# Kernel tuning notes

Hardware: AMD Instinct MI355X
Metric: run time of the kernel (lower is better)

The kernel has to match this reference:

```python
import jax, jax.numpy as jnp
import numpy as np

N = 100000
E = 1600000
DIN = 128
DH = 128
DOUT = 32
G = 64
EPS = 1e-5


def setup_inputs() -> dict:
    key = jax.random.key(0)
    ks = jax.random.split(key, 12)
    x = jax.random.normal(ks[0], (N, DIN), dtype=jnp.float32)
    edge_index = jax.random.randint(ks[1], (2, E), 0, N, dtype=jnp.int64)
    batch = jnp.sort(jax.random.randint(ks[2], (N,), 0, G, dtype=jnp.int64))
    # GCNConv weights (glorot-ish) + zero bias
    W1 = jax.random.normal(ks[3], (DIN, DH), dtype=jnp.float32) * (2.0 / (DIN + DH)) ** 0.5
    b1 = jnp.zeros((DH,), jnp.float32)
    W2 = jax.random.normal(ks[4], (DH, DH), dtype=jnp.float32) * (2.0 / (DH + DH)) ** 0.5
    b2 = jnp.zeros((DH,), jnp.float32)
    # BatchNorm affine params
    g1 = jnp.ones((DH,), jnp.float32); be1 = jnp.zeros((DH,), jnp.float32)
    g2 = jnp.ones((DH,), jnp.float32); be2 = jnp.zeros((DH,), jnp.float32)
    # Linear heads: kaiming normal fan_in relu, bias=0.001
    fw1 = jax.random.normal(ks[5], (DH, DH), dtype=jnp.float32) * (2.0 / DH) ** 0.5
    fb1 = jnp.full((DH,), 0.001, jnp.float32)
    fw2 = jax.random.normal(ks[6], (DH, DOUT), dtype=jnp.float32) * (2.0 / DH) ** 0.5
    fb2 = jnp.full((DOUT,), 0.001, jnp.float32)
    return dict(x=x, edge_index=edge_index, batch=batch, W1=W1, b1=b1, W2=W2, b2=b2,
                g1=g1, be1=be1, g2=g2, be2=be2, fw1=fw1, fb1=fb1, fw2=fw2, fb2=fb2)


def _gcn(x, src, dst, dinv, W, b):
    h = x @ W  # [N, F]
    norm = dinv[src] * dinv[dst]  # [E+N]
    agg = jax.ops.segment_sum(h[src] * norm[:, None], dst, num_segments=N)
    return agg + b


def _bn(h, gamma, beta):
    mu = h.mean(axis=0)
    var = h.var(axis=0)  # biased, matches torch BN training mode
    return (h - mu) * jax.lax.rsqrt(var + EPS) * gamma + beta


def reference(x, edge_index, batch, W1, b1, W2, b2, g1, be1, g2, be2, fw1, fb1, fw2, fb2):
    # add self-loops (PyG GCNConv default)
    loops = jnp.arange(N, dtype=edge_index.dtype)
    src = jnp.concatenate([edge_index[0], loops])
    dst = jnp.concatenate([edge_index[1], loops])
    deg = jax.ops.segment_sum(jnp.ones_like(dst, dtype=x.dtype), dst, num_segments=N)
    dinv = jnp.where(deg > 0, jax.lax.rsqrt(deg), 0.0)

    h = jax.nn.relu(_bn(_gcn(x, src, dst, dinv, W1, b1), g1, be1))
    h = jax.nn.relu(_bn(_gcn(h, src, dst, dinv, W2, b2), g2, be2))

    # global mean pool over graph ids
    sums = jax.ops.segment_sum(h, batch, num_segments=G)
    cnt = jax.ops.segment_sum(jnp.ones((N,), h.dtype), batch, num_segments=G)
    pooled = sums / jnp.maximum(cnt, 1.0)[:, None]  # [G, DH]

    z = jax.nn.relu(pooled @ fw1 + fb1)
    return jax.nn.softmax(z @ fw2 + fb2, axis=1)
```

## Files before the change

### kernel.cpp

```cpp
#include <hip/hip_runtime.h>
#include <hip/hip_bf16.h>
#include <stdint.h>

#define NN 100000
#define NE 1600000
#define DH 128
#define DOUT 32
#define NG 64
#define EPS 1e-5f

#define SCAN_BLK 1024
#define SCAN_NB ((NN + SCAN_BLK - 1) / SCAN_BLK)
#define NBUCKET 32
#define NRANGE 8
#define RANGE_SZ (NN / NRANGE)

#define PREP_COUNT_BLKS 1024
#define PREP_GB_BLKS ((NN + 255) / 256)
#define PREP_PW_BLKS 128

#define AGG_BLOCKS 4096
#define NCHUNK 32768

typedef __attribute__((ext_vector_type(8))) unsigned short ushort8;
typedef __attribute__((ext_vector_type(8))) short bfv8;
typedef __attribute__((ext_vector_type(4))) float f32x4;
typedef __attribute__((ext_vector_type(4))) int intv4;
typedef __attribute__((ext_vector_type(2))) unsigned int uintv2;

__device__ __forceinline__ float b2f(unsigned short u) {
    return __uint_as_float(((unsigned int)u) << 16);
}
__device__ __forceinline__ unsigned int f2b(float f) {
    unsigned int u = __float_as_uint(f);
    return (u + 0x7fffu + ((u >> 16) & 1u)) >> 16;
}
__device__ __forceinline__ float blo(unsigned int v) { return __uint_as_float(v << 16); }
__device__ __forceinline__ float bhi(unsigned int v) { return __uint_as_float(v & 0xffff0000u); }


__global__ void k_prep(const int* __restrict__ ei_dst, int* __restrict__ cnt,
                       const int* __restrict__ batch, int* __restrict__ gfirst, int* __restrict__ glast,
                       const float* __restrict__ W1, const float* __restrict__ W2,
                       unsigned short* __restrict__ WT1, unsigned short* __restrict__ WT2) {
    int bid = blockIdx.x;
    int t = threadIdx.x;
    if (bid < PREP_COUNT_BLKS) {
        int range = bid & (NRANGE - 1);
        int lo = range * RANGE_SZ, hi = lo + RANGE_SZ;
        int i = (bid >> 3) * 256 + t;
        int stride = (PREP_COUNT_BLKS >> 3) * 256;
        const intv4* d4 = reinterpret_cast<const intv4*>(ei_dst);
        for (int e = i; e < NE / 4; e += stride) {
            intv4 d = __builtin_nontemporal_load(d4 + e);
            if (d.x >= lo && d.x < hi) atomicAdd(&cnt[d.x], 1);
            if (d.y >= lo && d.y < hi) atomicAdd(&cnt[d.y], 1);
            if (d.z >= lo && d.z < hi) atomicAdd(&cnt[d.z], 1);
            if (d.w >= lo && d.w < hi) atomicAdd(&cnt[d.w], 1);
        }
    } else if (bid < PREP_COUNT_BLKS + PREP_GB_BLKS) {
        int i = (bid - PREP_COUNT_BLKS) * 256 + t;
        if (i < NN) {
            int g = batch[i];
            if (i == 0 || batch[i - 1] != g) gfirst[g] = i;
            if (i == NN - 1 || batch[i + 1] != g) glast[g] = i + 1;
        }
    } else {
        int i = (bid - PREP_COUNT_BLKS - PREP_GB_BLKS) * 256 + t;
        int sel = i >> 14;
        int j = i & 16383;
        int k = j >> 7, n = j & 127;
        const float* W = sel ? W2 : W1;
        unsigned short* WT = sel ? WT2 : WT1;
        WT[n * 128 + k] = (unsigned short)f2b(W[j]);
    }
}


__global__ void k_scan_partial(const int* __restrict__ cnt, int* __restrict__ bsum) {
    __shared__ int sdata[256];
    int blk = blockIdx.x, t = threadIdx.x;
    int base = blk * SCAN_BLK + t * 4;
    int s = 0;
#pragma unroll
    for (int q = 0; q < 4; q++) { int idx = base + q; if (idx < NN) s += cnt[idx]; }
    sdata[t] = s; __syncthreads();
    for (int o = 128; o; o >>= 1) { if (t < o) sdata[t] += sdata[t + o]; __syncthreads(); }
    if (t == 0) bsum[blk] = sdata[0];
}

__global__ void k_scan_final(int* __restrict__ cnt, const int* __restrict__ bsum,
                             int* __restrict__ rowptr, float* __restrict__ dinv,
                             const int* __restrict__ first, const int* __restrict__ last,
                             int* __restrict__ gcnt) {
    __shared__ int sdata[256];
    __shared__ int stop[128];
    __shared__ int sbase;
    int blk = blockIdx.x, t = threadIdx.x;

    if (t < 128) stop[t] = (t < SCAN_NB) ? bsum[t] : 0;
    __syncthreads();
    for (int o = 1; o < 128; o <<= 1) {
        int add = (t < 128 && t >= o) ? stop[t - o] : 0;
        __syncthreads();
        if (t < 128) stop[t] += add;
        __syncthreads();
    }
    if (t == 0) sbase = (blk > 0) ? stop[blk - 1] : 0;
    if (blk == 0) {
        if (t == 127) rowptr[NN] = stop[127];
        if (t < NG) gcnt[t] = last[t] - first[t];
    }
    __syncthreads();

    int base = blk * SCAN_BLK + t * 4;
    int v[4]; int s = 0;
#pragma unroll
    for (int q = 0; q < 4; q++) { int idx = base + q; v[q] = (idx < NN) ? cnt[idx] : 0; s += v[q]; }
    sdata[t] = s; __syncthreads();
    for (int o = 1; o < 256; o <<= 1) {
        int add = (t >= o) ? sdata[t - o] : 0;
        __syncthreads();
        sdata[t] += add;
        __syncthreads();
    }
    int offset = sbase + sdata[t] - s;
#pragma unroll
    for (int q = 0; q < 4; q++) {
        int idx = base + q;
        if (idx < NN) {
            rowptr[idx] = offset;
            cnt[idx] = offset;
            dinv[idx] = rsqrtf((float)(v[q] + 1));
            offset += v[q];
        }
    }
}

__global__ void k_fill(const int* __restrict__ ei, int* __restrict__ cursor, int* __restrict__ csr) {
    int range = blockIdx.x & (NRANGE - 1);
    int lo = range * RANGE_SZ, hi = lo + RANGE_SZ;
    int i = (blockIdx.x >> 3) * blockDim.x + threadIdx.x;
    int stride = (gridDim.x >> 3) * blockDim.x;
    const intv4* s4 = reinterpret_cast<const intv4*>(ei);
    const intv4* d4 = reinterpret_cast<const intv4*>(ei + NE);
    for (int e = i; e < NE / 4; e += stride) {
        intv4 s = __builtin_nontemporal_load(s4 + e);
        intv4 d = __builtin_nontemporal_load(d4 + e);
        if (d.x >= lo && d.x < hi) csr[atomicAdd(&cursor[d.x], 1)] = s.x;
        if (d.y >= lo && d.y < hi) csr[atomicAdd(&cursor[d.y], 1)] = s.y;
        if (d.z >= lo && d.z < hi) csr[atomicAdd(&cursor[d.z], 1)] = s.z;
        if (d.w >= lo && d.w < hi) csr[atomicAdd(&cursor[d.w], 1)] = s.w;
    }
}


template <bool BN, typename AT>
__global__ __launch_bounds__(256) void k_gemm(const AT* __restrict__ A, const unsigned short* __restrict__ WTg,
                                              unsigned short* __restrict__ C, const float* __restrict__ rowscale,
                                              const float* __restrict__ scale, const float* __restrict__ shift) {
    __shared__ unsigned char lds[65536];
    unsigned char* As = lds;
    unsigned char* Ws = lds + 32768;
    int row0 = blockIdx.x * 128;
    int t = threadIdx.x;
    int l = t & 63;
    int w = t >> 6;

    if constexpr (sizeof(AT) == 4) {
#pragma unroll
        for (int q = 0; q < 16; q++) {
            int idx = q * 256 + t;
            int r = idx >> 5, c4 = idx & 31;
            float4 v = make_float4(0.f, 0.f, 0.f, 0.f);
            if (row0 + r < NN) v = reinterpret_cast<const float4*>(A)[(size_t)(row0 + r) * 32 + c4];
            ushort4 u;
            u.x = (unsigned short)f2b(v.x);
            u.y = (unsigned short)f2b(v.y);
            u.z = (unsigned short)f2b(v.z);
            u.w = (unsigned short)f2b(v.w);
            int off = r * 256 + ((c4 * 8) ^ ((r & 7) << 4));
            *reinterpret_cast<ushort4*>(As + off) = u;
        }
    } else {
#pragma unroll
        for (int q = 0; q < 8; q++) {
            int idx = q * 256 + t;
            int r = idx >> 4, c8 = idx & 15;
            ushort8 v = (ushort8)0;
            if (row0 + r < NN) v = reinterpret_cast<const ushort8*>(A)[(size_t)(row0 + r) * 16 + c8];
            ushort8 u;
#pragma unroll
            for (int j = 0; j < 8; j++) {
                float f = b2f(v[j]);
                if (BN) { int k = c8 * 8 + j; f = fmaxf(f * scale[k] + shift[k], 0.f); }
                u[j] = (unsigned short)f2b(f);
            }
            int off = r * 256 + ((c8 * 16) ^ ((r & 7) << 4));
            *reinterpret_cast<ushort8*>(As + off) = u;
        }
    }
#pragma unroll
    for (int q = 0; q < 8; q++) {
        int idx = q * 256 + t;
        int n = idx >> 4, c8 = idx & 15;
        ushort8 v = reinterpret_cast<const ushort8*>(WTg)[idx];
        int off = n * 256 + ((c8 * 16) ^ ((n & 7) << 4));
        *reinterpret_cast<ushort8*>(Ws + off) = v;
    }
    __syncthreads();

    f32x4 acc[2][8];
#pragma unroll
    for (int m = 0; m < 2; m++)
#pragma unroll
        for (int n = 0; n < 8; n++) acc[m][n] = (f32x4)0.f;

    int lrow = l & 15;
    int kbyte0 = (l >> 4) * 16;
#pragma unroll
    for (int kt = 0; kt < 4; kt++) {
        int kb = kt * 64 + kbyte0;
        bfv8 a[2];
#pragma unroll
        for (int m = 0; m < 2; m++) {
            int r = w * 32 + m * 16 + lrow;
            a[m] = *reinterpret_cast<const bfv8*>(As + r * 256 + (kb ^ ((r & 7) << 4)));
        }
        bfv8 b[8];
#pragma unroll
        for (int n = 0; n < 8; n++) {
            int r = n * 16 + lrow;
            b[n] = *reinterpret_cast<const bfv8*>(Ws + r * 256 + (kb ^ ((r & 7) << 4)));
        }
#pragma unroll
        for (int m = 0; m < 2; m++)
#pragma unroll
            for (int n = 0; n < 8; n++)
                acc[m][n] = __builtin_amdgcn_mfma_f32_16x16x32_bf16(a[m], b[n], acc[m][n], 0, 0, 0);
    }

#pragma unroll
    for (int m = 0; m < 2; m++) {
#pragma unroll
        for (int rr = 0; rr < 4; rr++) {
            int grow = row0 + w * 32 + m * 16 + (l >> 4) * 4 + rr;
            if (grow < NN) {
                float rs = rowscale[grow];
#pragma unroll
                for (int n = 0; n < 8; n++) {
                    int col = n * 16 + (l & 15);
                    C[(size_t)grow * DH + col] = (unsigned short)f2b(acc[m][n][rr] * rs);
                }
            }
        }
    }
}


__global__ __launch_bounds__(128) void k_aggregate(const unsigned short* __restrict__ h, const int* __restrict__ rowptr,
                                                   const int* __restrict__ csr, const float* __restrict__ dinv,
                                                   unsigned short* __restrict__ agg, float* __restrict__ stats) {
    int lane = threadIdx.x & 63;
    int wv = threadIdx.x >> 6;
    int half = lane >> 5;
    int sl = lane & 31;
    const uintv2* h64 = reinterpret_cast<const uintv2*>(h);
    uintv2* agg64 = reinterpret_cast<uintv2*>(agg);
    int wid = blockIdx.x * 2 + wv;
    int nw = gridDim.x * 2;

    float s0 = 0.f, s1 = 0.f, s2 = 0.f, s3 = 0.f;
    float q0 = 0.f, q1 = 0.f, q2 = 0.f, q3 = 0.f;

    for (int c = wid; c < NCHUNK; c += nw) {
        long long tlo = ((long long)c * NE) / NCHUNK;
        long long thi = (c == NCHUNK - 1) ? (long long)NE + 1 : (((long long)(c + 1) * NE) / NCHUNK);
        int thii = (int)thi;

        int lo = 0, hi = NN;
        while (lo < hi) {
            int mid = (lo + hi) >> 1;
            if (rowptr[mid] < (int)tlo) lo = mid + 1; else hi = mid;
        }

        for (int i = lo; i < NN; i++) {
            int row = rowptr[i];
            if (row >= thii) break;
            int end = rowptr[i + 1];
            int len = end - row;
            float di = dinv[i];
            float a0 = 0.f, a1 = 0.f, a2 = 0.f, a3 = 0.f;
            if (half == 0) {
                uintv2 sv = h64[(size_t)i * 32 + sl];
                a0 = blo(sv.x); a1 = bhi(sv.x); a2 = blo(sv.y); a3 = bhi(sv.y);
            }
            int hc = (len + 1 - half) >> 1;
            int tt = 0;
            for (; tt + 4 <= hc; tt += 4) {
                int eA = row + (tt << 1) + half;
                int n0 = csr[eA], n1 = csr[eA + 2], n2 = csr[eA + 4], n3 = csr[eA + 6];
                uintv2 v0 = h64[(size_t)n0 * 32 + sl];
                uintv2 v1 = h64[(size_t)n1 * 32 + sl];
                uintv2 v2 = h64[(size_t)n2 * 32 + sl];
                uintv2 v3 = h64[(size_t)n3 * 32 + sl];
                a0 += blo(v0.x); a1 += bhi(v0.x); a2 += blo(v0.y); a3 += bhi(v0.y);
                a0 += blo(v1.x); a1 += bhi(v1.x); a2 += blo(v1.y); a3 += bhi(v1.y);
                a0 += blo(v2.x); a1 += bhi(v2.x); a2 += blo(v2.y); a3 += bhi(v2.y);
                a0 += blo(v3.x); a1 += bhi(v3.x); a2 += blo(v3.y); a3 += bhi(v3.y);
            }
            for (; tt < hc; tt++) {
                int e = row + (tt << 1) + half;
                int n = csr[e];
                uintv2 v = h64[(size_t)n * 32 + sl];
                a0 += blo(v.x); a1 += bhi(v.x); a2 += blo(v.y); a3 += bhi(v.y);
            }
            a0 += __shfl_xor(a0, 32);
            a1 += __shfl_xor(a1, 32);
            a2 += __shfl_xor(a2, 32);
            a3 += __shfl_xor(a3, 32);
            a0 *= di; a1 *= di; a2 *= di; a3 *= di;
            if (half == 0) {
                uintv2 o;
                o.x = f2b(a0) | (f2b(a1) << 16);
                o.y = f2b(a2) | (f2b(a3) << 16);
                agg64[(size_t)i * 32 + sl] = o;
                s0 += a0; q0 += a0 * a0;
                s1 += a1; q1 += a1 * a1;
                s2 += a2; q2 += a2 * a2;
                s3 += a3; q3 += a3 * a3;
            }
        }
    }

    if (half == 0) {
        float* b = stats + (size_t)(wid & (NBUCKET - 1)) * 256;
        atomicAdd(&b[sl * 4 + 0], s0);
        atomicAdd(&b[sl * 4 + 1], s1);
        atomicAdd(&b[sl * 4 + 2], s2);
        atomicAdd(&b[sl * 4 + 3], s3);
        atomicAdd(&b[128 + sl * 4 + 0], q0);
        atomicAdd(&b[128 + sl * 4 + 1], q1);
        atomicAdd(&b[128 + sl * 4 + 2], q2);
        atomicAdd(&b[128 + sl * 4 + 3], q3);
    }
}

__global__ void k_bnparams(const float* __restrict__ stats, const float* __restrict__ gamma,
                           const float* __restrict__ beta, float* __restrict__ scale, float* __restrict__ shift) {
    int j = threadIdx.x;
    float su = 0.f, sq = 0.f;
    for (int b = 0; b < NBUCKET; b++) { su += stats[b * 256 + j]; sq += stats[b * 256 + 128 + j]; }
    float mu = su * (1.f / NN);
    float var = sq * (1.f / NN) - mu * mu;
    float rs = rsqrtf(var + EPS);
    float sc = rs * gamma[j];
    scale[j] = sc;
    shift[j] = beta[j] - mu * sc;
}


#define POOL_CHUNK 256

__global__ __launch_bounds__(256) void k_pool(const unsigned short* __restrict__ agg, const int* __restrict__ batch,
                                              const float* __restrict__ stats, const float* __restrict__ gamma,
                                              const float* __restrict__ beta, float* __restrict__ pooled) {
    __shared__ float s_sc[DH], s_sh[DH];
    int t = threadIdx.x;
    if (t < DH) {
        float su = 0.f, sq = 0.f;
        for (int b = 0; b < NBUCKET; b++) { su += stats[b * 256 + t]; sq += stats[b * 256 + 128 + t]; }
        float mu = su * (1.f / NN);
        float var = sq * (1.f / NN) - mu * mu;
        float rs = rsqrtf(var + EPS);
        float sc = rs * gamma[t];
        s_sc[t] = sc;
        s_sh[t] = beta[t] - mu * sc;
    }
    __syncthreads();

    int half = t >> 5;
    int sl = t & 31;
    int n0 = blockIdx.x * POOL_CHUNK + half * 32;
    if (n0 >= NN) return;
    int n1 = n0 + 32; if (n1 > NN) n1 = NN;

    const uintv2* a64 = reinterpret_cast<const uintv2*>(agg);
    float sc0 = s_sc[sl * 4 + 0], sh0 = s_sh[sl * 4 + 0];
    float sc1 = s_sc[sl * 4 + 1], sh1 = s_sh[sl * 4 + 1];
    float sc2 = s_sc[sl * 4 + 2], sh2 = s_sh[sl * 4 + 2];
    float sc3 = s_sc[sl * 4 + 3], sh3 = s_sh[sl * 4 + 3];

    int gcur = batch[n0];
    float a0 = 0.f, a1 = 0.f, a2 = 0.f, a3 = 0.f;
    for (int i = n0; i < n1; i++) {
        int g = batch[i];
        if (g != gcur) {
            atomicAdd(&pooled[(size_t)gcur * DH + sl * 4 + 0], a0);
            atomicAdd(&pooled[(size_t)gcur * DH + sl * 4 + 1], a1);
            atomicAdd(&pooled[(size_t)gcur * DH + sl * 4 + 2], a2);
            atomicAdd(&pooled[(size_t)gcur * DH + sl * 4 + 3], a3);
            a0 = a1 = a2 = a3 = 0.f; gcur = g;
        }
        uintv2 v = a64[(size_t)i * 32 + sl];
        a0 += fmaxf(blo(v.x) * sc0 + sh0, 0.f);
        a1 += fmaxf(bhi(v.x) * sc1 + sh1, 0.f);
        a2 += fmaxf(blo(v.y) * sc2 + sh2, 0.f);
        a3 += fmaxf(bhi(v.y) * sc3 + sh3, 0.f);
    }
    atomicAdd(&pooled[(size_t)gcur * DH + sl * 4 + 0], a0);
    atomicAdd(&pooled[(size_t)gcur * DH + sl * 4 + 1], a1);
    atomicAdd(&pooled[(size_t)gcur * DH + sl * 4 + 2], a2);
    atomicAdd(&pooled[(size_t)gcur * DH + sl * 4 + 3], a3);
}


__global__ __launch_bounds__(128) void k_head(const float* __restrict__ pooled, const int* __restrict__ gcnt,
                                              const float* __restrict__ fw1, const float* __restrict__ fb1,
                                              const float* __restrict__ fw2, const float* __restrict__ fb2,
                                              float* __restrict__ out) {
    __shared__ float p[DH];
    __shared__ float z[DH];
    int g = blockIdx.x;
    int j = threadIdx.x;
    float cnt = (float)max(gcnt[g], 1);
    p[j] = pooled[(size_t)g * DH + j] / cnt;
    __syncthreads();
    float a = fb1[j];
    for (int k = 0; k < DH; k++) a += p[k] * fw1[k * DH + j];
    z[j] = fmaxf(a, 0.f);
    __syncthreads();
    if (j < DOUT) {
        float l = fb2[j];
        for (int k = 0; k < DH; k++) l += z[k] * fw2[k * DOUT + j];
        float m = l;
        for (int o = 16; o; o >>= 1) m = fmaxf(m, __shfl_xor(m, o, 32));
        float e = expf(l - m);
        float s = e;
        for (int o = 16; o; o >>= 1) s += __shfl_xor(s, o, 32);
        out[(size_t)g * DOUT + j] = e / s;
    }
}


static inline char* align256p(char* p) {
    return (char*)(((uintptr_t)p + 255) & ~(uintptr_t)255);
}

extern "C" void kernel_launch(void* const* d_in, const int* in_sizes, int n_in,
                              void* d_out, int out_size, void* d_ws, size_t ws_size,
                              hipStream_t stream) {
    const float* x     = (const float*)d_in[0];
    const int*   ei    = (const int*)d_in[1];
    const int*   batch = (const int*)d_in[2];
    const float* W1    = (const float*)d_in[3];
    const float* W2    = (const float*)d_in[5];
    const float* g1    = (const float*)d_in[7];
    const float* be1   = (const float*)d_in[8];
    const float* g2    = (const float*)d_in[9];
    const float* be2   = (const float*)d_in[10];
    const float* fw1   = (const float*)d_in[11];
    const float* fb1   = (const float*)d_in[12];
    const float* fw2   = (const float*)d_in[13];
    const float* fb2   = (const float*)d_in[14];
    float* out = (float*)d_out;

    char* w = (char*)d_ws;
    unsigned short* hbuf = (unsigned short*)w;  w += (size_t)NN * DH * 2;
    unsigned short* abuf = (unsigned short*)w;  w += (size_t)NN * DH * 2;
    int*   csr    = (int*)w;    w += (size_t)NE * 4;
    int*   rowptr = (int*)w;    w += (size_t)(NN + 1) * 4;  w = align256p(w);
    float* dinv   = (float*)w;  w += (size_t)NN * 4;
    int*   bsum   = (int*)w;    w += 512 * 4;
    float* scale1 = (float*)w;  w += DH * 4;
    float* shift1 = (float*)w;  w += DH * 4;
    unsigned short* WT1g = (unsigned short*)w;  w += (size_t)DH * DH * 2;
    unsigned short* WT2g = (unsigned short*)w;  w += (size_t)DH * DH * 2;
    w = align256p(w);
    char* zstart  = w;
    int*   cnt    = (int*)w;    w += (size_t)NN * 4;
    int*   gfirst = (int*)w;    w += 64 * 4;
    int*   glast  = (int*)w;    w += 64 * 4;
    int*   gcnt   = (int*)w;    w += 64 * 4;
    float* stats1 = (float*)w;  w += (size_t)NBUCKET * 256 * 4;
    float* stats2 = (float*)w;  w += (size_t)NBUCKET * 256 * 4;
    float* pooled = (float*)w;  w += (size_t)NG * DH * 4;
    size_t zbytes = (size_t)(w - zstart);
    size_t need = (size_t)(w - (char*)d_ws);
    if (ws_size < need) return;

    hipMemsetAsync(zstart, 0, zbytes, stream);

    k_prep<<<PREP_COUNT_BLKS + PREP_GB_BLKS + PREP_PW_BLKS, 256, 0, stream>>>(
        ei + NE, cnt, batch, gfirst, glast, W1, W2, WT1g, WT2g);
    k_scan_partial<<<SCAN_NB, 256, 0, stream>>>(cnt, bsum);
    k_scan_final<<<SCAN_NB, 256, 0, stream>>>(cnt, bsum, rowptr, dinv, gfirst, glast, gcnt);
    k_fill<<<1024, 256, 0, stream>>>(ei, cnt, csr);

    int gemm_grid = (NN + 127) / 128;

    k_gemm<false, float><<<gemm_grid, 256, 0, stream>>>(x, WT1g, hbuf, dinv, nullptr, nullptr);
    k_aggregate<<<AGG_BLOCKS, 128, 0, stream>>>(hbuf, rowptr, csr, dinv, abuf, stats1);
    k_bnparams<<<1, 128, 0, stream>>>(stats1, g1, be1, scale1, shift1);

    k_gemm<true, unsigned short><<<gemm_grid, 256, 0, stream>>>(abuf, WT2g, hbuf, dinv, scale1, shift1);
    k_aggregate<<<AGG_BLOCKS, 128, 0, stream>>>(hbuf, rowptr, csr, dinv, abuf, stats2);

    int pool_grid = (NN + POOL_CHUNK - 1) / POOL_CHUNK;
    k_pool<<<pool_grid, 256, 0, stream>>>(abuf, batch, stats2, g2, be2, pooled);
    k_head<<<NG, 128, 0, stream>>>(pooled, gcnt, fw1, fb1, fw2, fb2, out);
}
```

Before: 449.0 us.

## Fold BN parameter computation into GEMM, halve edge range partitions, drop nontemporal loads

Removes the separate single-block k_bnparams launch. Each BN-enabled GEMM block now reduces the stats buckets itself and keeps scale and shift in shared memory, which also replaces per-element global loads of scale and shift with LDS reads. Separately, the counting and CSR-fill kernels split destinations into 4 ranges instead of 8, so the edge arrays are read fewer times, and they switch from nontemporal to ordinary loads. The cost is redundant stats reduction in every GEMM block and more atomic contention per range.

```diff
diff --git a/kernel.cpp b/kernel.cpp
--- a/kernel.cpp
+++ b/kernel.cpp
@@ -12,7 +12,7 @@
 #define SCAN_BLK 1024
 #define SCAN_NB ((NN + SCAN_BLK - 1) / SCAN_BLK)
 #define NBUCKET 32
-#define NRANGE 8
+#define NRANGE 4
 #define RANGE_SZ (NN / NRANGE)
 
 #define PREP_COUNT_BLKS 1024
@@ -48,11 +48,11 @@
     if (bid < PREP_COUNT_BLKS) {
         int range = bid & (NRANGE - 1);
         int lo = range * RANGE_SZ, hi = lo + RANGE_SZ;
-        int i = (bid >> 3) * 256 + t;
-        int stride = (PREP_COUNT_BLKS >> 3) * 256;
+        int i = (bid >> 2) * 256 + t;
+        int stride = (PREP_COUNT_BLKS >> 2) * 256;
         const intv4* d4 = reinterpret_cast<const intv4*>(ei_dst);
         for (int e = i; e < NE / 4; e += stride) {
-            intv4 d = __builtin_nontemporal_load(d4 + e);
+            intv4 d = d4[e];
             if (d.x >= lo && d.x < hi) atomicAdd(&cnt[d.x], 1);
             if (d.y >= lo && d.y < hi) atomicAdd(&cnt[d.y], 1);
             if (d.z >= lo && d.z < hi) atomicAdd(&cnt[d.z], 1);
@@ -140,13 +140,13 @@
 __global__ void k_fill(const int* __restrict__ ei, int* __restrict__ cursor, int* __restrict__ csr) {
     int range = blockIdx.x & (NRANGE - 1);
     int lo = range * RANGE_SZ, hi = lo + RANGE_SZ;
-    int i = (blockIdx.x >> 3) * blockDim.x + threadIdx.x;
-    int stride = (gridDim.x >> 3) * blockDim.x;
+    int i = (blockIdx.x >> 2) * blockDim.x + threadIdx.x;
+    int stride = (gridDim.x >> 2) * blockDim.x;
     const intv4* s4 = reinterpret_cast<const intv4*>(ei);
     const intv4* d4 = reinterpret_cast<const intv4*>(ei + NE);
     for (int e = i; e < NE / 4; e += stride) {
-        intv4 s = __builtin_nontemporal_load(s4 + e);
-        intv4 d = __builtin_nontemporal_load(d4 + e);
+        intv4 s = s4[e];
+        intv4 d = d4[e];
         if (d.x >= lo && d.x < hi) csr[atomicAdd(&cursor[d.x], 1)] = s.x;
         if (d.y >= lo && d.y < hi) csr[atomicAdd(&cursor[d.y], 1)] = s.y;
         if (d.z >= lo && d.z < hi) csr[atomicAdd(&cursor[d.z], 1)] = s.z;
@@ -158,14 +158,30 @@
 template <bool BN, typename AT>
 __global__ __launch_bounds__(256) void k_gemm(const AT* __restrict__ A, const unsigned short* __restrict__ WTg,
                                               unsigned short* __restrict__ C, const float* __restrict__ rowscale,
-                                              const float* __restrict__ scale, const float* __restrict__ shift) {
+                                              const float* __restrict__ stats, const float* __restrict__ gamma,
+                                              const float* __restrict__ beta) {
     __shared__ unsigned char lds[65536];
+    __shared__ float s_sc[DH], s_sh[DH];
     unsigned char* As = lds;
     unsigned char* Ws = lds + 32768;
     int row0 = blockIdx.x * 128;
     int t = threadIdx.x;
     int l = t & 63;
     int w = t >> 6;
+
+    if constexpr (BN) {
+        if (t < DH) {
+            float su = 0.f, sq = 0.f;
+            for (int b = 0; b < NBUCKET; b++) { su += stats[b * 256 + t]; sq += stats[b * 256 + 128 + t]; }
+            float mu = su * (1.f / NN);
+            float var = sq * (1.f / NN) - mu * mu;
+            float rs = rsqrtf(var + EPS);
+            float sc = rs * gamma[t];
+            s_sc[t] = sc;
+            s_sh[t] = beta[t] - mu * sc;
+        }
+        __syncthreads();
+    }
 
     if constexpr (sizeof(AT) == 4) {
 #pragma unroll
@@ -193,7 +209,7 @@
 #pragma unroll
             for (int j = 0; j < 8; j++) {
                 float f = b2f(v[j]);
-                if (BN) { int k = c8 * 8 + j; f = fmaxf(f * scale[k] + shift[k], 0.f); }
+                if (BN) { int k = c8 * 8 + j; f = fmaxf(f * s_sc[k] + s_sh[k], 0.f); }
                 u[j] = (unsigned short)f2b(f);
             }
             int off = r * 256 + ((c8 * 16) ^ ((r & 7) << 4));
@@ -346,19 +362,6 @@
     }
 }
 
-__global__ void k_bnparams(const float* __restrict__ stats, const float* __restrict__ gamma,
-                           const float* __restrict__ beta, float* __restrict__ scale, float* __restrict__ shift) {
-    int j = threadIdx.x;
-    float su = 0.f, sq = 0.f;
-    for (int b = 0; b < NBUCKET; b++) { su += stats[b * 256 + j]; sq += stats[b * 256 + 128 + j]; }
-    float mu = su * (1.f / NN);
-    float var = sq * (1.f / NN) - mu * mu;
-    float rs = rsqrtf(var + EPS);
-    float sc = rs * gamma[j];
-    scale[j] = sc;
-    shift[j] = beta[j] - mu * sc;
-}
-
 
 #define POOL_CHUNK 256
 
@@ -472,8 +475,6 @@
     int*   rowptr = (int*)w;    w += (size_t)(NN + 1) * 4;  w = align256p(w);
     float* dinv   = (float*)w;  w += (size_t)NN * 4;
     int*   bsum   = (int*)w;    w += 512 * 4;
-    float* scale1 = (float*)w;  w += DH * 4;
-    float* shift1 = (float*)w;  w += DH * 4;
     unsigned short* WT1g = (unsigned short*)w;  w += (size_t)DH * DH * 2;
     unsigned short* WT2g = (unsigned short*)w;  w += (size_t)DH * DH * 2;
     w = align256p(w);
@@ -499,11 +500,10 @@
 
     int gemm_grid = (NN + 127) / 128;
 
-    k_gemm<false, float><<<gemm_grid, 256, 0, stream>>>(x, WT1g, hbuf, dinv, nullptr, nullptr);
+    k_gemm<false, float><<<gemm_grid, 256, 0, stream>>>(x, WT1g, hbuf, dinv, nullptr, nullptr, nullptr);
     k_aggregate<<<AGG_BLOCKS, 128, 0, stream>>>(hbuf, rowptr, csr, dinv, abuf, stats1);
-    k_bnparams<<<1, 128, 0, stream>>>(stats1, g1, be1, scale1, shift1);
-
-    k_gemm<true, unsigned short><<<gemm_grid, 256, 0, stream>>>(abuf, WT2g, hbuf, dinv, scale1, shift1);
+
+    k_gemm<true, unsigned short><<<gemm_grid, 256, 0, stream>>>(abuf, WT2g, hbuf, dinv, stats1, g1, be1);
     k_aggregate<<<AGG_BLOCKS, 128, 0, stream>>>(hbuf, rowptr, csr, dinv, abuf, stats2);
 
     int pool_grid = (NN + POOL_CHUNK - 1) / POOL_CHUNK;
```

Measured after the change: 442.7 us. Within noise of the previous version (-1.4%).
